# Performance work log

Hardware: AMD Instinct MI355X
Metric: run time of the kernel (lower is better)

## Reference

```python
import jax, jax.numpy as jnp
import numpy as np

B, H, W, C = 32, 56, 56, 256
NH, WS, SHIFT = 8, 7, 3
S = WS * WS            # tokens per window = 49
CH = C // NH           # channels per head = 32
EPS = 1e-5


def layer_norm(x, w, b):
    mu = jnp.mean(x, axis=-1, keepdims=True)
    var = jnp.var(x, axis=-1, keepdims=True)
    return (x - mu) * jax.lax.rsqrt(var + EPS) * w + b


def spatial_mlp(x, weight, bias):
    # x: (B, H*W, C); weight: (NH*S, S, 1) grouped-conv1d weight; bias: (NH*S,)
    xr = x.reshape(B, H, W, C)
    if SHIFT > 0:
        P_l, P_r, P_t, P_b = WS - SHIFT, SHIFT, WS - SHIFT, SHIFT
        xr = jnp.pad(xr, ((0, 0), (P_t, P_b), (P_l, P_r), (0, 0)))
    Hp, Wp = xr.shape[1], xr.shape[2]
    # window partition -> (nW, S, NH, CH)
    win = xr.reshape(B, Hp // WS, WS, Wp // WS, WS, C)
    win = win.transpose(0, 1, 3, 2, 4, 5).reshape(-1, S, NH, CH)
    # grouped 1x1 conv == per-head token-mixing matrix (S x S)
    wgt = weight.reshape(NH, S, S)             # wgt[h, i, j]
    out = jnp.einsum('hij,njhd->nihd', wgt, win)
    out = out + bias.reshape(NH, S).T[None, :, :, None]
    # window reverse -> (B, Hp, Wp, C)
    out = out.reshape(B, Hp // WS, Wp // WS, WS, WS, C)
    out = out.transpose(0, 1, 3, 2, 4, 5).reshape(B, Hp, Wp, C)
    if SHIFT > 0:
        out = out[:, P_t:Hp - P_b, P_l:Wp - P_r, :]
    return out.reshape(B, H * W, C)


def mlp(x, fc1_w, fc1_b, fc2_w, fc2_b):
    h = jax.nn.gelu(x @ fc1_w + fc1_b, approximate=False)
    return h @ fc2_w + fc2_b


def setup_inputs() -> dict:
    key = jax.random.key(0)
    ks = jax.random.split(key, 5)
    sc = 0.02
    return {
        'x': jax.random.normal(ks[0], (B, H * W, C), jnp.float32),
        'norm1_w': jnp.ones((C,), jnp.float32),
        'norm1_b': jnp.zeros((C,), jnp.float32),
        'spatial_w': jax.random.normal(ks[1], (NH * S, S, 1), jnp.float32) * sc,
        'spatial_b': jax.random.normal(ks[2], (NH * S,), jnp.float32) * sc,
        'norm2_w': jnp.ones((C,), jnp.float32),
        'norm2_b': jnp.zeros((C,), jnp.float32),
        'fc1_w': jax.random.normal(ks[3], (C, 4 * C), jnp.float32) * sc,
        'fc1_b': jnp.zeros((4 * C,), jnp.float32),
        'fc2_w': jax.random.normal(ks[4], (4 * C, C), jnp.float32) * sc,
        'fc2_b': jnp.zeros((C,), jnp.float32),
    }


def reference(x, norm1_w, norm1_b, spatial_w, spatial_b, norm2_w, norm2_b,
              fc1_w, fc1_b, fc2_w, fc2_b):
    shortcut = x
    h = layer_norm(x, norm1_w, norm1_b)
    h = spatial_mlp(h, spatial_w, spatial_b)
    x = shortcut + h                      # drop_path = 0 (eval)
    x = x + mlp(layer_norm(x, norm2_w, norm2_b), fc1_w, fc1_b, fc2_w, fc2_b)
    return x
```

## Files before the change

### kernel.cpp

```cpp
#include <hip/hip_runtime.h>
#include <hip/hip_bf16.h>

#define NHEAD 8
#define IMG   3136
#define MTOT  100352

typedef __attribute__((ext_vector_type(2))) _Float16 f16x2;
typedef __attribute__((ext_vector_type(4))) float    f32x4;
typedef __attribute__((ext_vector_type(16))) float   f32x16;
typedef __attribute__((ext_vector_type(8))) short    bf16x8;
typedef __attribute__((ext_vector_type(2))) int      i32x2;
typedef __attribute__((ext_vector_type(4))) int      i32x4;

#define SWZA(byteoff, r) ((byteoff) ^ (((r)&7)<<4) ^ ((((r)>>3)&1)<<7))
#define SWZC(byteoff, r) ((byteoff) ^ (((r)&7)<<4) ^ ((((r)>>3)&1)<<7))

__device__ __forceinline__ short f2bf(float f){
  union { float fv; unsigned u; } a; a.fv = f;
  unsigned u = a.u;
  unsigned r = (u + 0x7fffu + ((u >> 16) & 1u)) >> 16;
  return (short)r;
}

__device__ __forceinline__ unsigned cvtpk(float lo, float hi){
  unsigned r;
  asm("v_cvt_pk_bf16_f32 %0, %1, %2" : "=v"(r) : "v"(lo), "v"(hi));
  return r;
}

__device__ __forceinline__ float gelu_s(float v){
  float e = __expf(-1.702f*v);
  return v*__builtin_amdgcn_rcpf(1.f + e);
}

__global__ void prep_k(const float* __restrict__ fc1w, const float* __restrict__ fc2w,
                       const float* __restrict__ spw,
                       short* __restrict__ w1p, short* __restrict__ w2p,
                       short* __restrict__ wspA)
{
  int bid = blockIdx.x, t = threadIdx.x;
  if (bid < 128) {
    int id = bid*256 + t;
    int l = id & 63, fk = id >> 6;
    int kk = fk & 15, f = fk >> 4;
    int n = f*32 + (l & 31);
    int kbase = kk*16 + (l >> 5)*8;
    bf16x8 o;
    #pragma unroll
    for (int e = 0; e < 8; ++e) o[e] = f2bf(fc1w[(size_t)(kbase+e)*1024 + n]);
    *(bf16x8*)(w1p + (size_t)id*8) = o;
  } else if (bid < 256) {
    int id = (bid-128)*256 + t;
    int l = id & 63, fk = id >> 6;
    int kk = fk & 63, f = fk >> 6;
    int n = f*32 + (l & 31);
    int kbase = kk*16 + (l >> 5)*8;
    bf16x8 o;
    #pragma unroll
    for (int e = 0; e < 8; ++e) o[e] = f2bf(fc2w[(size_t)(kbase+e)*256 + n]);
    *(bf16x8*)(w2p + (size_t)id*8) = o;
  } else {
    #pragma unroll
    for (int k = 0; k < 16; ++k) {
      int idx = t + k*256;
      int lane = idx & 63;
      int kt = (idx >> 6) & 3;
      int mt = (idx >> 8) & 1;
      int h  = idx >> 9;
      int i  = mt*32 + (lane & 31);
      int jb = kt*16 + (lane >> 5)*8;
      bf16x8 o;
      #pragma unroll
      for (int e = 0; e < 8; ++e) {
        int j = jb + e;
        float v = (i < 49 && j < 49) ? spw[(size_t)(h*49 + i)*49 + j] : 0.f;
        o[e] = f2bf(v);
      }
      *(bf16x8*)(wspA + (size_t)idx*8) = o;
    }
  }
}

__global__ __launch_bounds__(512,4) void win_k(
    const float* __restrict__ x, const float* __restrict__ n1w, const float* __restrict__ n1b,
    const float* __restrict__ spb, const short* __restrict__ wspA,
    float* __restrict__ x1)
{
  extern __shared__ char wsm[];
  char*  lxT  = wsm;
  float* murs = (float*)(wsm + 65536);
  int t = threadIdx.x, lane = t & 63, wave = t >> 6;
  int bid = blockIdx.x;

  #pragma unroll
  for (int w = 0; w < 2; ++w) {
    int win = bid*2 + w;
    int b = win/81, rem = win - b*81, wi = rem/9, wj = rem - (rem/9)*9;
    for (int i = wave; i < 49; i += 8) {
      int iy = i/7, ix = i - iy*7;
      int hh = wi*7 + iy - 4, ww = wj*7 + ix - 4;
      if (hh < 0 || hh >= 56 || ww < 0 || ww >= 56) continue;
      const float* row = x + ((size_t)(b*IMG + hh*56 + ww))*256;
      f32x4 v = *(const f32x4*)(row + lane*4);
      float s  = v[0]+v[1]+v[2]+v[3];
      float s2 = v[0]*v[0]+v[1]*v[1]+v[2]*v[2]+v[3]*v[3];
      #pragma unroll
      for (int m = 1; m < 64; m <<= 1) { s += __shfl_xor(s, m); s2 += __shfl_xor(s2, m); }
      float mu = s * (1.f/256.f);
      float rs = rsqrtf(s2*(1.f/256.f) - mu*mu + 1e-5f);
      if (lane == 0) { murs[(w*56+i)*2] = mu; murs[(w*56+i)*2+1] = rs; }
    }
  }
  __syncthreads();

  {
    int w = t >> 8, c = t & 255;
    int win = bid*2 + w;
    int b = win/81, rem = win - b*81, wi = rem/9, wj = rem - (rem/9)*9;
    float nwc = n1w[c], nbc = n1b[c];
    char* rowb = lxT + c*256;
    #pragma unroll
    for (int cj = 0; cj < 7; ++cj) {
      float vals[8];
      #pragma unroll
      for (int e = 0; e < 8; ++e) {
        int p = cj*8 + e;
        float fv = 0.f;
        if (p < 49) {
          int iy = p/7, ix = p - iy*7;
          int hh = wi*7 + iy - 4, ww = wj*7 + ix - 4;
          if (hh >= 0 && hh < 56 && ww >= 0 && ww < 56) {
            float mu = murs[(w*56+p)*2], rs = murs[(w*56+p)*2+1];
            float xv = x[((size_t)(b*IMG + hh*56 + ww))*256 + c];
            fv = (xv - mu)*rs*nwc + nbc;
          }
        }
        vals[e] = fv;
      }
      i32x4 pk;
      pk[0] = cvtpk(vals[0], vals[1]); pk[1] = cvtpk(vals[2], vals[3]);
      pk[2] = cvtpk(vals[4], vals[5]); pk[3] = cvtpk(vals[6], vals[7]);
      *(i32x4*)(rowb + SWZA(w*128 + cj*16, c)) = pk;
    }
    i32x4 z = {0,0,0,0};
    *(i32x4*)(rowb + SWZA(w*128 + 112, c)) = z;
  }
  __syncthreads();

  int h = wave, d = lane & 31, lk = lane >> 5;
  const short* wA = wspA + h*4096;
  int c = h*32 + d;
  f32x16 a00, a01, a10, a11;
  #pragma unroll
  for (int q = 0; q < 16; ++q) { a00[q]=0.f; a01[q]=0.f; a10[q]=0.f; a11[q]=0.f; }
  #pragma unroll
  for (int kt = 0; kt < 4; ++kt) {
    bf16x8 A0 = *(const bf16x8*)(wA + (kt*64 + lane)*8);
    bf16x8 A1 = *(const bf16x8*)(wA + ((4+kt)*64 + lane)*8);
    int bo = kt*32 + lk*16;
    bf16x8 B0 = *(const bf16x8*)(lxT + c*256 + SWZA(bo, c));
    bf16x8 B1 = *(const bf16x8*)(lxT + c*256 + SWZA(128 + bo, c));
    a00 = __builtin_amdgcn_mfma_f32_32x32x16_bf16(A0, B0, a00, 0,0,0);
    a10 = __builtin_amdgcn_mfma_f32_32x32x16_bf16(A1, B0, a10, 0,0,0);
    a01 = __builtin_amdgcn_mfma_f32_32x32x16_bf16(A0, B1, a01, 0,0,0);
    a11 = __builtin_amdgcn_mfma_f32_32x32x16_bf16(A1, B1, a11, 0,0,0);
  }

  #pragma unroll
  for (int w = 0; w < 2; ++w) {
    int win = bid*2 + w;
    int b = win/81, rem = win - b*81, wi = rem/9, wj = rem - (rem/9)*9;
    #pragma unroll
    for (int mt = 0; mt < 2; ++mt) {
      #pragma unroll
      for (int r = 0; r < 16; ++r) {
        int i = mt*32 + (r&3) + 8*(r>>2) + 4*lk;
        if (i < 49) {
          int iy = i/7, ix = i - iy*7;
          int hh = wi*7 + iy - 4, ww = wj*7 + ix - 4;
          if (hh >= 0 && hh < 56 && ww >= 0 && ww < 56) {
            size_t off = ((size_t)(b*IMG + hh*56 + ww))*256 + c;
            float av = mt==0 ? (w==0 ? a00[r] : a01[r]) : (w==0 ? a10[r] : a11[r]);
            x1[off] = x[off] + av + spb[h*49 + i];
          }
        }
      }
    }
  }
}

__global__ __launch_bounds__(256,4) void mlp_k(
    const float* __restrict__ x1, float* __restrict__ out,
    const short* __restrict__ w1p, const short* __restrict__ w2p,
    const float* __restrict__ n2w, const float* __restrict__ n2b,
    const float* __restrict__ b1, const float* __restrict__ b2)
{
  extern __shared__ char sm[];
  char* a2  = sm;
  char* hc0 = sm + 16384;
  char* hc1 = sm + 24576;

  int t = threadIdx.x, lane = t & 63, wave = t >> 6;
  int m0 = blockIdx.x * 32;
  int lr = lane & 31, lk = lane >> 5;
  int wn = wave;

  const short* g1 = w1p + ((size_t)(wn*16)*64 + lane)*8;
  const short* g2 = w2p + ((size_t)((wn*2)*64)*64 + lane)*8;

  bf16x8 bq[4];
  #pragma unroll
  for (int k = 0; k < 4; ++k) bq[k] = *(const bf16x8*)(g1 + (size_t)k*512);

  {
    f32x4 nw = *(const f32x4*)(n2w + lane*4);
    f32x4 nb = *(const f32x4*)(n2b + lane*4);
    #pragma unroll
    for (int rq = 0; rq < 8; ++rq) {
      int rr = wave*8 + rq;
      f32x4 v = *(const f32x4*)(x1 + (size_t)(m0+rr)*256 + lane*4);
      float s  = v[0]+v[1]+v[2]+v[3];
      float s2 = v[0]*v[0]+v[1]*v[1]+v[2]*v[2]+v[3]*v[3];
      #pragma unroll
      for (int m = 1; m < 64; m <<= 1){ s += __shfl_xor(s,m); s2 += __shfl_xor(s2,m); }
      float mu = s*(1.f/256.f);
      float rs = rsqrtf(s2*(1.f/256.f) - mu*mu + 1e-5f);
      float y0 = (v[0]-mu)*rs*nw[0] + nb[0];
      float y1 = (v[1]-mu)*rs*nw[1] + nb[1];
      float y2 = (v[2]-mu)*rs*nw[2] + nb[2];
      float y3 = (v[3]-mu)*rs*nw[3] + nb[3];
      i32x2 pk; pk[0] = cvtpk(y0,y1); pk[1] = cvtpk(y2,y3);
      *(i32x2*)(a2 + SWZA(lane*8, rr) + rr*512) = pk;
    }
  }
  __syncthreads();

  f32x16 accO[2];
  #pragma unroll
  for (int i=0;i<2;++i)
    #pragma unroll
    for (int q=0;q<16;++q) accO[i][q] = 0.f;

  for (int ch = 0; ch < 8; ++ch) {
    f32x16 accH;
    #pragma unroll
    for (int q=0;q<16;++q) accH[q] = 0.f;

    __builtin_amdgcn_s_setprio(1);
    #pragma unroll
    for (int kk = 0; kk < 16; ++kk) {
      bf16x8 b = bq[kk & 3];
      if (kk < 12) bq[kk & 3] = *(const bf16x8*)(g1 + (size_t)(kk+4)*512);
      int kb = kk*32 + lk*16;
      bf16x8 a0 = *(const bf16x8*)(a2 + SWZA(kb, lr) + lr*512);
      accH = __builtin_amdgcn_mfma_f32_32x32x16_bf16(a0, b, accH, 0,0,0);
    }
    __builtin_amdgcn_s_setprio(0);

    bq[0] = *(const bf16x8*)(g2 + (size_t)0*512);
    bq[1] = *(const bf16x8*)(g2 + (size_t)64*512);
    bq[2] = *(const bf16x8*)(g2 + (size_t)1*512);
    bq[3] = *(const bf16x8*)(g2 + (size_t)65*512);

    char* hcw = (ch & 1) ? hc1 : hc0;

    {
      float b1v = b1[ch*128 + wn*32 + lr];
      int colb = (wn*32 + lr)*2;
      #pragma unroll
      for (int r2 = 0; r2 < 8; ++r2) {
        int r = r2*2;
        float g0 = gelu_s(accH[r]   + b1v);
        float g1v = gelu_s(accH[r+1] + b1v);
        unsigned pw = cvtpk(g0, g1v);
        int row0 = (r&3) + 8*(r>>2) + 4*lk;
        int row1 = row0 + 1;
        *(short*)(hcw + SWZC(colb, row0) + row0*256) = (short)(pw & 0xffffu);
        *(short*)(hcw + SWZC(colb, row1) + row1*256) = (short)(pw >> 16);
      }
    }
    __syncthreads();

    __builtin_amdgcn_s_setprio(1);
    #pragma unroll
    for (int kk = 0; kk < 8; ++kk) {
      bf16x8 b0, b1f;
      if ((kk&1)==0) { b0 = bq[0]; b1f = bq[1]; } else { b0 = bq[2]; b1f = bq[3]; }
      if (kk < 6) {
        bf16x8 n0 = *(const bf16x8*)(g2 + (size_t)(kk+2)*512);
        bf16x8 n1 = *(const bf16x8*)(g2 + (size_t)(64+kk+2)*512);
        if ((kk&1)==0) { bq[0] = n0; bq[1] = n1; } else { bq[2] = n0; bq[3] = n1; }
      }
      int kb = kk*32 + lk*16;
      bf16x8 a0 = *(const bf16x8*)(hcw + SWZC(kb, lr) + lr*256);
      accO[0] = __builtin_amdgcn_mfma_f32_32x32x16_bf16(a0, b0, accO[0], 0,0,0);
      accO[1] = __builtin_amdgcn_mfma_f32_32x32x16_bf16(a0, b1f, accO[1], 0,0,0);
    }
    __builtin_amdgcn_s_setprio(0);

    g1 += (size_t)64*512;
    g2 += (size_t)8*512;
    if (ch < 7) {
      #pragma unroll
      for (int k = 0; k < 4; ++k) bq[k] = *(const bf16x8*)(g1 + (size_t)k*512);
    }
  }

  #pragma unroll
  for (int ns = 0; ns < 2; ++ns) {
    int col = wn*64 + ns*32 + lr;
    float b2v = b2[col];
    #pragma unroll
    for (int r = 0; r < 16; ++r) {
      int row = (r&3) + 8*(r>>2) + 4*lk;
      size_t off = (size_t)(m0 + row)*256 + col;
      float av = ns==0 ? accO[0][r] : accO[1][r];
      out[off] = x1[off] + av + b2v;
    }
  }
}

extern "C" void kernel_launch(void* const* d_in, const int* in_sizes, int n_in,
                              void* d_out, int out_size, void* d_ws, size_t ws_size,
                              hipStream_t stream) {
  const float* x    = (const float*)d_in[0];
  const float* n1w  = (const float*)d_in[1];
  const float* n1b  = (const float*)d_in[2];
  const float* spw  = (const float*)d_in[3];
  const float* spb  = (const float*)d_in[4];
  const float* n2w  = (const float*)d_in[5];
  const float* n2b  = (const float*)d_in[6];
  const float* fc1w = (const float*)d_in[7];
  const float* fc1b = (const float*)d_in[8];
  const float* fc2w = (const float*)d_in[9];
  const float* fc2b = (const float*)d_in[10];
  float* outp = (float*)d_out;

  char* ws = (char*)d_ws;
  short* w1p  = (short*)ws;
  short* w2p  = (short*)(ws + 524288);
  short* wspA = (short*)(ws + 1048576);

  prep_k<<<257, 256, 0, stream>>>(fc1w, fc2w, spw, w1p, w2p, wspA);

  hipFuncSetAttribute(reinterpret_cast<const void*>(win_k),
                      hipFuncAttributeMaxDynamicSharedMemorySize, 66432);
  win_k<<<1296, 512, 66432, stream>>>(x, n1w, n1b, spb, wspA, outp);

  hipFuncSetAttribute(reinterpret_cast<const void*>(mlp_k),
                      hipFuncAttributeMaxDynamicSharedMemorySize, 32768);
  mlp_k<<<MTOT/32, 256, 32768, stream>>>(outp, outp, w1p, w2p, n2w, n2b, fc1b, fc2b);
}
```

Before: 302.5 us.

## Double MLP row tile to 64 and software-pipeline fc2 of previous chunk into fc1

The MLP kernel now handles 64 rows per block with 8 waves (two row groups by four column groups), so each weight fragment fetched from global memory serves twice as many rows. The fc2 MFMAs for the previous hidden chunk are interleaved into the fc1 loop of the current chunk through double-buffered hidden tiles, which removes one barrier per chunk and overlaps the two GEMMs. The cost is more shared memory (64 KB per block) and more registers per thread, which may lower occupancy. The LayerNorm prologue still appears to use wave*8 rows, so with 8 waves it should cover all 64 rows.

After: 376.1 us. +24.3%, slower.

```diff
diff --git a/kernel.cpp b/kernel.cpp
--- a/kernel.cpp
+++ b/kernel.cpp
@@ -189,7 +189,7 @@
   }
 }
 
-__global__ __launch_bounds__(256,4) void mlp_k(
+__global__ __launch_bounds__(512,4) void mlp_k(
     const float* __restrict__ x1, float* __restrict__ out,
     const short* __restrict__ w1p, const short* __restrict__ w2p,
     const float* __restrict__ n2w, const float* __restrict__ n2b,
@@ -197,20 +197,21 @@
 {
   extern __shared__ char sm[];
   char* a2  = sm;
-  char* hc0 = sm + 16384;
-  char* hc1 = sm + 24576;
+  char* hc0 = sm + 32768;
+  char* hc1 = sm + 49152;
 
   int t = threadIdx.x, lane = t & 63, wave = t >> 6;
-  int m0 = blockIdx.x * 32;
+  int m0 = blockIdx.x * 64;
   int lr = lane & 31, lk = lane >> 5;
-  int wn = wave;
+  int wm = wave >> 2, wn = wave & 3;
+  int arow = wm*32 + lr;
 
   const short* g1 = w1p + ((size_t)(wn*16)*64 + lane)*8;
   const short* g2 = w2p + ((size_t)((wn*2)*64)*64 + lane)*8;
 
-  bf16x8 bq[4];
-  #pragma unroll
-  for (int k = 0; k < 4; ++k) bq[k] = *(const bf16x8*)(g1 + (size_t)k*512);
+  bf16x8 bq1[4], bq2[4];
+  #pragma unroll
+  for (int k = 0; k < 4; ++k) bq1[k] = *(const bf16x8*)(g1 + (size_t)k*512);
 
   {
     f32x4 nw = *(const f32x4*)(n2w + lane*4);
@@ -235,34 +236,89 @@
   }
   __syncthreads();
 
-  f32x16 accO[2];
-  #pragma unroll
-  for (int i=0;i<2;++i)
-    #pragma unroll
-    for (int q=0;q<16;++q) accO[i][q] = 0.f;
-
-  for (int ch = 0; ch < 8; ++ch) {
-    f32x16 accH;
+  f32x16 accO0, accO1;
+  #pragma unroll
+  for (int q=0;q<16;++q) { accO0[q] = 0.f; accO1[q] = 0.f; }
+
+  f32x16 accH;
+  #pragma unroll
+  for (int q=0;q<16;++q) accH[q] = 0.f;
+
+  __builtin_amdgcn_s_setprio(1);
+  #pragma unroll
+  for (int kk = 0; kk < 16; ++kk) {
+    bf16x8 b = bq1[kk & 3];
+    if (kk < 12) bq1[kk & 3] = *(const bf16x8*)(g1 + (size_t)(kk+4)*512);
+    bf16x8 a = *(const bf16x8*)(a2 + SWZA(kk*32 + lk*16, arow) + arow*512);
+    accH = __builtin_amdgcn_mfma_f32_32x32x16_bf16(a, b, accH, 0,0,0);
+  }
+  __builtin_amdgcn_s_setprio(0);
+
+  bq2[0] = *(const bf16x8*)(g2 + (size_t)0);
+  bq2[1] = *(const bf16x8*)(g2 + (size_t)32768);
+  bq2[2] = *(const bf16x8*)(g2 + (size_t)512);
+  bq2[3] = *(const bf16x8*)(g2 + (size_t)32768 + 512);
+  g1 += 32768;
+  #pragma unroll
+  for (int k = 0; k < 4; ++k) bq1[k] = *(const bf16x8*)(g1 + (size_t)k*512);
+
+  {
+    float b1v = b1[wn*32 + lr];
+    int colb = (wn*32 + lr)*2;
+    #pragma unroll
+    for (int r2 = 0; r2 < 8; ++r2) {
+      int r = r2*2;
+      float g0 = gelu_s(accH[r]   + b1v);
+      float g1v = gelu_s(accH[r+1] + b1v);
+      unsigned pw = cvtpk(g0, g1v);
+      int row0 = wm*32 + (r&3) + 8*(r>>2) + 4*lk;
+      int row1 = row0 + 1;
+      *(short*)(hc0 + SWZC(colb, row0) + row0*256) = (short)(pw & 0xffffu);
+      *(short*)(hc0 + SWZC(colb, row1) + row1*256) = (short)(pw >> 16);
+    }
+  }
+  __syncthreads();
+
+  for (int ch = 1; ch < 8; ++ch) {
+    char* hcprev = (ch & 1) ? hc0 : hc1;
+    char* hcw    = (ch & 1) ? hc1 : hc0;
+
     #pragma unroll
     for (int q=0;q<16;++q) accH[q] = 0.f;
 
     __builtin_amdgcn_s_setprio(1);
     #pragma unroll
     for (int kk = 0; kk < 16; ++kk) {
-      bf16x8 b = bq[kk & 3];
-      if (kk < 12) bq[kk & 3] = *(const bf16x8*)(g1 + (size_t)(kk+4)*512);
-      int kb = kk*32 + lk*16;
-      bf16x8 a0 = *(const bf16x8*)(a2 + SWZA(kb, lr) + lr*512);
-      accH = __builtin_amdgcn_mfma_f32_32x32x16_bf16(a0, b, accH, 0,0,0);
+      bf16x8 b = bq1[kk & 3];
+      if (kk < 12) bq1[kk & 3] = *(const bf16x8*)(g1 + (size_t)(kk+4)*512);
+      bf16x8 a = *(const bf16x8*)(a2 + SWZA(kk*32 + lk*16, arow) + arow*512);
+      accH = __builtin_amdgcn_mfma_f32_32x32x16_bf16(a, b, accH, 0,0,0);
+      if ((kk & 1) == 0) {
+        int kk2 = kk >> 1;
+        bf16x8 c0, c1;
+        if (kk2 & 1) { c0 = bq2[2]; c1 = bq2[3]; } else { c0 = bq2[0]; c1 = bq2[1]; }
+        if (kk2 < 6) {
+          bf16x8 n0 = *(const bf16x8*)(g2 + (size_t)(kk2+2)*512);
+          bf16x8 n1 = *(const bf16x8*)(g2 + (size_t)32768 + (size_t)(kk2+2)*512);
+          if (kk2 & 1) { bq2[2] = n0; bq2[3] = n1; } else { bq2[0] = n0; bq2[1] = n1; }
+        }
+        bf16x8 hfrag = *(const bf16x8*)(hcprev + SWZC(kk2*32 + lk*16, arow) + arow*256);
+        accO0 = __builtin_amdgcn_mfma_f32_32x32x16_bf16(hfrag, c0, accO0, 0,0,0);
+        accO1 = __builtin_amdgcn_mfma_f32_32x32x16_bf16(hfrag, c1, accO1, 0,0,0);
+      }
     }
     __builtin_amdgcn_s_setprio(0);
 
-    bq[0] = *(const bf16x8*)(g2 + (size_t)0*512);
-    bq[1] = *(const bf16x8*)(g2 + (size_t)64*512);
-    bq[2] = *(const bf16x8*)(g2 + (size_t)1*512);
-    bq[3] = *(const bf16x8*)(g2 + (size_t)65*512);
-
-    char* hcw = (ch & 1) ? hc1 : hc0;
+    g2 += 4096;
+    bq2[0] = *(const bf16x8*)(g2 + (size_t)0);
+    bq2[1] = *(const bf16x8*)(g2 + (size_t)32768);
+    bq2[2] = *(const bf16x8*)(g2 + (size_t)512);
+    bq2[3] = *(const bf16x8*)(g2 + (size_t)32768 + 512);
+    if (ch < 7) {
+      g1 += 32768;
+      #pragma unroll
+      for (int k = 0; k < 4; ++k) bq1[k] = *(const bf16x8*)(g1 + (size_t)k*512);
+    }
 
     {
       float b1v = b1[ch*128 + wn*32 + lr];
@@ -273,38 +329,30 @@
         float g0 = gelu_s(accH[r]   + b1v);
         float g1v = gelu_s(accH[r+1] + b1v);
         unsigned pw = cvtpk(g0, g1v);
-        int row0 = (r&3) + 8*(r>>2) + 4*lk;
+        int row0 = wm*32 + (r&3) + 8*(r>>2) + 4*lk;
         int row1 = row0 + 1;
         *(short*)(hcw + SWZC(colb, row0) + row0*256) = (short)(pw & 0xffffu);
         *(short*)(hcw + SWZC(colb, row1) + row1*256) = (short)(pw >> 16);
       }
     }
     __syncthreads();
-
-    __builtin_amdgcn_s_setprio(1);
-    #pragma unroll
-    for (int kk = 0; kk < 8; ++kk) {
-      bf16x8 b0, b1f;
-      if ((kk&1)==0) { b0 = bq[0]; b1f = bq[1]; } else { b0 = bq[2]; b1f = bq[3]; }
-      if (kk < 6) {
-        bf16x8 n0 = *(const bf16x8*)(g2 + (size_t)(kk+2)*512);
-        bf16x8 n1 = *(const bf16x8*)(g2 + (size_t)(64+kk+2)*512);
-        if ((kk&1)==0) { bq[0] = n0; bq[1] = n1; } else { bq[2] = n0; bq[3] = n1; }
-      }
-      int kb = kk*32 + lk*16;
-      bf16x8 a0 = *(const bf16x8*)(hcw + SWZC(kb, lr) + lr*256);
-      accO[0] = __builtin_amdgcn_mfma_f32_32x32x16_bf16(a0, b0, accO[0], 0,0,0);
-      accO[1] = __builtin_amdgcn_mfma_f32_32x32x16_bf16(a0, b1f, accO[1], 0,0,0);
-    }
-    __builtin_amdgcn_s_setprio(0);
-
-    g1 += (size_t)64*512;
-    g2 += (size_t)8*512;
-    if (ch < 7) {
-      #pragma unroll
-      for (int k = 0; k < 4; ++k) bq[k] = *(const bf16x8*)(g1 + (size_t)k*512);
-    }
-  }
+  }
+
+  __builtin_amdgcn_s_setprio(1);
+  #pragma unroll
+  for (int kk2 = 0; kk2 < 8; ++kk2) {
+    bf16x8 c0, c1;
+    if (kk2 & 1) { c0 = bq2[2]; c1 = bq2[3]; } else { c0 = bq2[0]; c1 = bq2[1]; }
+    if (kk2 < 6) {
+      bf16x8 n0 = *(const bf16x8*)(g2 + (size_t)(kk2+2)*512);
+      bf16x8 n1 = *(const bf16x8*)(g2 + (size_t)32768 + (size_t)(kk2+2)*512);
+      if (kk2 & 1) { bq2[2] = n0; bq2[3] = n1; } else { bq2[0] = n0; bq2[1] = n1; }
+    }
+    bf16x8 hfrag = *(const bf16x8*)(hc1 + SWZC(kk2*32 + lk*16, arow) + arow*256);
+    accO0 = __builtin_amdgcn_mfma_f32_32x32x16_bf16(hfrag, c0, accO0, 0,0,0);
+    accO1 = __builtin_amdgcn_mfma_f32_32x32x16_bf16(hfrag, c1, accO1, 0,0,0);
+  }
+  __builtin_amdgcn_s_setprio(0);
 
   #pragma unroll
   for (int ns = 0; ns < 2; ++ns) {
@@ -312,9 +360,9 @@
     float b2v = b2[col];
     #pragma unroll
     for (int r = 0; r < 16; ++r) {
-      int row = (r&3) + 8*(r>>2) + 4*lk;
+      int row = wm*32 + (r&3) + 8*(r>>2) + 4*lk;
       size_t off = (size_t)(m0 + row)*256 + col;
-      float av = ns==0 ? accO[0][r] : accO[1][r];
+      float av = ns==0 ? accO0[r] : accO1[r];
       out[off] = x1[off] + av + b2v;
     }
   }
@@ -348,6 +396,6 @@
   win_k<<<1296, 512, 66432, stream>>>(x, n1w, n1b, spb, wspA, outp);
 
   hipFuncSetAttribute(reinterpret_cast<const void*>(mlp_k),
-                      hipFuncAttributeMaxDynamicSharedMemorySize, 32768);
-  mlp_k<<<MTOT/32, 256, 32768, stream>>>(outp, outp, w1p, w2p, n2w, n2b, fc1b, fc2b);
-}
+                      hipFuncAttributeMaxDynamicSharedMemorySize, 65536);
+  mlp_k<<<MTOT/64, 512, 65536, stream>>>(outp, outp, w1p, w2p, n2w, n2b, fc1b, fc2b);
+}
```
